# Optimization experiments

Measured on AMD Instinct MI355X. Metric: run time of the kernel, lower is better.

The kernel has to match this reference:

```python
import jax, jax.numpy as jnp
import numpy as np
from jax import lax

B, W, L, E, V, C, H, O = 16384, 5, 20, 50, 100000, 128, 4096, 50


def setup_inputs() -> dict:
    key = jax.random.key(0)
    ks = jax.random.split(key, 10)
    x = jax.random.randint(ks[0], (B, W), 1, V)
    word_id_to_chars_ids = jax.random.randint(ks[1], (V, L), 0, C)
    word_emb = jax.random.normal(ks[2], (V, E), dtype=jnp.float32) * 0.1
    word_emb = word_emb.at[0].set(0.0)  # padding_idx=0
    char_emb = jax.random.normal(ks[3], (C, E), dtype=jnp.float32) * 0.1
    char_emb = char_emb.at[0].set(0.0)  # padding_idx=0
    conv_w = jax.random.normal(ks[4], (E, E, 3), dtype=jnp.float32) * (1.0 / np.sqrt(E * 3))
    conv_b = jax.random.normal(ks[5], (E,), dtype=jnp.float32) * 0.01
    fc1_w = jax.random.normal(ks[6], (H, E * W), dtype=jnp.float32) * (1.0 / np.sqrt(E * W))
    fc1_b = jnp.zeros((H,), dtype=jnp.float32)
    fc2_w = jax.random.normal(ks[7], (O, H), dtype=jnp.float32) * (1.0 / np.sqrt(H))
    fc2_b = jnp.zeros((O,), dtype=jnp.float32)
    return {"x": x, "word_id_to_chars_ids": word_id_to_chars_ids,
            "word_emb": word_emb, "char_emb": char_emb,
            "conv_w": conv_w, "conv_b": conv_b,
            "fc1_w": fc1_w, "fc1_b": fc1_b, "fc2_w": fc2_w, "fc2_b": fc2_b}


def reference(x, word_id_to_chars_ids, word_emb, char_emb, conv_w, conv_b,
              fc1_w, fc1_b, fc2_w, fc2_b):
    # per-window char ids: [B, 5, L] -> char embeddings [B, 5, L, E]
    char_ids = word_id_to_chars_ids[x]
    ce = char_emb[char_ids]
    # conv1d over char positions: reshape to NCW = [B*5, E, L]
    ce = ce.reshape(B * W, L, E).transpose(0, 2, 1)
    conv = lax.conv_general_dilated(ce, conv_w, window_strides=(1,),
                                    padding=[(1, 1)],
                                    dimension_numbers=("NCH", "OIH", "NCH"))
    conv = conv + conv_b[None, :, None]
    # max-pool over char positions (kernel == L): [B*5, E] -> [B, 5, E]
    chars = jnp.max(conv, axis=2).reshape(B, W, E)
    words = word_emb[x]  # [B, 5, E]
    h = (words + chars).reshape(B, W * E)  # view(-1, 250)
    h = jnp.tanh(h @ fc1_w.T + fc1_b)
    logits = h @ fc2_w.T + fc2_b
    return jax.nn.softmax(logits, axis=1)
```

## Files before the change

kernel.cpp:

```cpp
#include <hip/hip_runtime.h>
#include <hip/hip_bf16.h>


typedef __attribute__((ext_vector_type(8))) short short8;
typedef __attribute__((ext_vector_type(4))) float float4v;

__device__ inline short bf16b(float f) {
    __hip_bfloat16 h = __float2bfloat16(f);
    return *reinterpret_cast<short*>(&h);
}
__device__ inline uint packbf2(float a, float b) {
    return (uint)(ushort)bf16b(a) | ((uint)(ushort)bf16b(b) << 16);
}
__device__ inline void gload_lds16(const void* g, void* l) {
    __builtin_amdgcn_global_load_lds(
        (const __attribute__((address_space(1))) unsigned int*)g,
        (__attribute__((address_space(3))) unsigned int*)l, 16, 0, 0);
}

struct F3 { float x, y, z; };

__global__ __launch_bounds__(256) void prep_kernel(
    const float* __restrict__ fc1_w, const float* __restrict__ fc1_b,
    const float* __restrict__ fc2_w, const float* __restrict__ char_emb,
    const float* __restrict__ conv_w, short* __restrict__ wbf,
    short* __restrict__ w2bf, float* __restrict__ gt2,
    __hip_bfloat16* __restrict__ ha)
{
    const int bid = blockIdx.x;
    if (bid < 4096) {
        int idx = bid * 256 + threadIdx.x;
        int n = idx >> 8, k = idx & 255;
        float v = (k < 250) ? fc1_w[n * 250 + k] : (k == 250 ? fc1_b[n] : 0.f);
        int CT = n >> 4, mm = n & 15;
        int ks = k >> 5, qq = (k >> 3) & 3, j = k & 7;
        wbf[((CT * 8 + ks) * 64 + qq * 16 + mm) * 8 + j] = bf16b(v);
    } else if (bid < 5120) {
        int idx = (bid - 4096) * 256 + threadIdx.x;
        int o = idx >> 12, k = idx & 4095;
        float v = (o < 50) ? fc2_w[idx] : 0.f;
        int Ot = o >> 4, mm = o & 15;
        int kst = k >> 5, qq = (k >> 3) & 3, j = k & 7;
        w2bf[((kst * 4 + Ot) * 64 + qq * 16 + mm) * 8 + j] = bf16b(v);
    } else if (bid < 5195) {
        int idx = (bid - 5120) * 256 + threadIdx.x;
        if (idx >= 19200) return;
        int c = idx / 150, rem = idx - c * 150;
        int kk = rem / 50, o = rem - kk * 50;
        const float* ce = char_emb + c * 50;
        const float* w  = conv_w + o * 150 + kk;
        float s = 0.f;
        #pragma unroll 10
        for (int i = 0; i < 50; ++i) s += ce[i] * w[i * 3];
        gt2[(c * 50 + o) * 3 + kk] = s;
    } else {
        int idx = (bid - 5195) * 256 + threadIdx.x;
        int b = idx / 6, j = idx - b * 6;
        ha[b * 256 + 250 + j] = __float2bfloat16(j == 0 ? 1.f : 0.f);
    }
}

__global__ __launch_bounds__(512, 4) void conv_kernel(
    const int* __restrict__ x, const int* __restrict__ wci,
    const float* __restrict__ word_emb, const float* __restrict__ conv_b,
    const float* __restrict__ gt2, __hip_bfloat16* __restrict__ ha)
{
    __shared__ float Gs[19200];
    __shared__ uint  cpack[640];
    __shared__ int   xs[128];
    char* gsb = (char*)Gs;

    const int tid = threadIdx.x;
    const int gw0 = blockIdx.x * 128;

    #pragma unroll
    for (int t = 0; t < 38; ++t) {
        int idx = t * 512 + tid;
        if (idx < 19200) Gs[idx] = gt2[idx];
    }

    if (tid < 128) {
        const int xid = x[gw0 + tid];
        xs[tid] = xid;
        const int* crow = wci + (size_t)xid * 20;
        int cid[20];
        #pragma unroll
        for (int p = 0; p < 20; ++p) cid[p] = crow[p];
        #pragma unroll
        for (int u = 0; u < 5; ++u)
            cpack[tid * 5 + u] = (uint)cid[u * 4] | ((uint)cid[u * 4 + 1] << 8)
                               | ((uint)cid[u * 4 + 2] << 16) | ((uint)cid[u * 4 + 3] << 24);
    }
    __syncthreads();

    const int lane = tid & 63;
    const int wv   = tid >> 6;
    const int oc   = (lane < 50) ? lane : 49;
    const int oc12 = oc * 12;
    const float cbias = conv_b[oc];

    for (int it = 0; it < 16; ++it) {
        const int wl = it * 8 + wv;
        uint cw[5];
        #pragma unroll
        for (int u = 0; u < 5; ++u) cw[u] = cpack[wl * 5 + u];
        const int xid = xs[wl];

        int cb[20];
        #pragma unroll
        for (int p = 0; p < 20; ++p) {
            const int c = (int)((cw[p >> 2] >> ((p & 3) * 8)) & 0xFF);
            cb[p] = c * 600 + oc12;
        }

        F3 r[11];
        #pragma unroll
        for (int l = 0; l < 11; ++l) r[l] = *(const F3*)(gsb + cb[l]);

        float mx = r[0].y + r[1].z;
        #pragma unroll
        for (int l = 1; l < 10; ++l) {
            float s = r[l].y + r[l - 1].x + r[l + 1].z;
            mx = fmaxf(mx, s);
        }
        const F3 r9 = r[9], r10 = r[10];

        F3 qv[9];
        #pragma unroll
        for (int l = 0; l < 9; ++l) qv[l] = *(const F3*)(gsb + cb[11 + l]);

        {
            float s = r10.y + r9.x + qv[0].z;
            mx = fmaxf(mx, s);
        }
        {
            float s = qv[0].y + r10.x + qv[1].z;
            mx = fmaxf(mx, s);
        }
        #pragma unroll
        for (int l = 12; l < 19; ++l) {
            float s = qv[l - 11].y + qv[l - 12].x + qv[l - 10].z;
            mx = fmaxf(mx, s);
        }
        {
            float s = qv[8].y + qv[7].x;
            mx = fmaxf(mx, s);
        }

        const float wer = word_emb[(size_t)xid * 50 + oc];
        const float res = mx + cbias + wer;
        const int gw = gw0 + wl;
        const int b = gw / 5, wp = gw - b * 5;
        if (lane < 50)
            ha[b * 256 + wp * 50 + lane] = __float2bfloat16(res);
    }
}

__global__ __launch_bounds__(512, 1) void fused_kernel(
    const __hip_bfloat16* __restrict__ ha, const short* __restrict__ wbf,
    const short* __restrict__ w2bf, float* __restrict__ gpart)
{
    __shared__ char smem[147456];
    short8* Bsv = (short8*)smem;
    char*   hsb = smem + 131072;
    float*  partf = (float*)smem;

    const int tid  = threadIdx.x;
    const int lane = tid & 63;
    const int wv   = tid >> 6;
    const int wr = wv >> 2, wc = wv & 3;
    const int q = lane >> 4, m = lane & 15;
    const int rg = blockIdx.x >> 1, kh = blockIdx.x & 1;
    const int m0 = rg * 64;
    const int q2base = q >> 1, slot = q & 1;

    const short8* wbfv  = (const short8*)wbf;
    const short8* w2bfv = (const short8*)w2bf;
    const short8* hav   = (const short8*)ha;

    short8 av[2][8];
    #pragma unroll
    for (int mt = 0; mt < 2; ++mt)
        #pragma unroll
        for (int ks = 0; ks < 8; ++ks)
            av[mt][ks] = hav[(size_t)(m0 + wr * 32 + mt * 16 + m) * 32 + ks * 4 + q];
    #pragma unroll
    for (int mt = 0; mt < 2; ++mt)
        #pragma unroll
        for (int ks = 0; ks < 8; ++ks)
            asm volatile("" : "+v"(av[mt][ks]));

    #pragma unroll
    for (int i = 0; i < 8; ++i)
        gload_lds16(wbfv + (size_t)(kh * 16) * 4096 + i * 512 + tid,
                    Bsv + i * 512 + tid);
    __syncthreads();

    float4v acc2[2][4] = {};

    #pragma unroll 4
    for (int chl = 0; chl < 16; ++chl) {
        const int buf = chl & 1;
        const int chg = kh * 16 + chl;

        short8 b2[4];
        #pragma unroll
        for (int Ot = 0; Ot < 4; ++Ot)
            b2[Ot] = w2bfv[(size_t)((chg * 4 + wc) * 4 + Ot) * 64 + lane];

        #pragma unroll
        for (int i = 0; i < 8; ++i)
            gload_lds16(wbfv + (size_t)(chg + 1) * 4096 + i * 512 + tid,
                        Bsv + (buf ^ 1) * 4096 + i * 512 + tid);

        float4v acc[2][2] = {};
        #pragma unroll
        for (int ks = 0; ks < 8; ++ks) {
            short8 bv[2];
            #pragma unroll
            for (int nt = 0; nt < 2; ++nt)
                bv[nt] = Bsv[buf * 4096 + ((wc * 2 + nt) * 8 + ks) * 64 + lane];
            #pragma unroll
            for (int mt = 0; mt < 2; ++mt)
                #pragma unroll
                for (int nt = 0; nt < 2; ++nt)
                    acc[mt][nt] = __builtin_amdgcn_mfma_f32_16x16x32_bf16(
                        bv[nt], av[mt][ks], acc[mt][nt], 0, 0, 0);
        }

        #pragma unroll
        for (int mt = 0; mt < 2; ++mt) {
            const int frag = (wr * 2 + mt) * 4 + wc;
            #pragma unroll
            for (int nt = 0; nt < 2; ++nt) {
                float tv[4];
                #pragma unroll
                for (int r = 0; r < 4; ++r)
                    tv[r] = 1.f - 2.f / (__expf(2.f * acc[mt][nt][r]) + 1.f);
                const int q2 = nt * 2 + q2base;
                const uint p0 = packbf2(tv[0], tv[1]);
                const uint p1 = packbf2(tv[2], tv[3]);
                *(uint2*)(hsb + ((frag * 64 + q2 * 16 + m) * 16 + slot * 8))
                    = make_uint2(p0, p1);
            }
        }

        {
            short8 a2[2];
            #pragma unroll
            for (int mt = 0; mt < 2; ++mt)
                a2[mt] = *(const short8*)(hsb
                    + (((wr * 2 + mt) * 4 + wc) * 64 + lane) * 16);
            #pragma unroll
            for (int mt = 0; mt < 2; ++mt)
                #pragma unroll
                for (int Ot = 0; Ot < 4; ++Ot)
                    acc2[mt][Ot] = __builtin_amdgcn_mfma_f32_16x16x32_bf16(
                        a2[mt], b2[Ot], acc2[mt][Ot], 0, 0, 0);
        }

        __syncthreads();
    }

    #pragma unroll
    for (int mt = 0; mt < 2; ++mt)
        #pragma unroll
        for (int Ot = 0; Ot < 4; ++Ot)
            #pragma unroll
            for (int r = 0; r < 4; ++r)
                partf[(size_t)wc * 4096
                      + ((wr * 2 + mt) * 16 + q * 4 + r) * 64 + Ot * 16 + m]
                    = acc2[mt][Ot][r];
    __syncthreads();

    #pragma unroll
    for (int t = 0; t < 8; ++t) {
        int idx = t * 512 + tid;
        float s = partf[idx] + partf[4096 + idx]
                + partf[8192 + idx] + partf[12288 + idx];
        gpart[(size_t)blockIdx.x * 4096 + idx] = s;
    }
}

__global__ __launch_bounds__(256) void combine_kernel(
    const float* __restrict__ gpart, const float* __restrict__ fc2_b,
    float* __restrict__ out)
{
    const int tid  = threadIdx.x;
    const int lane = tid & 63;
    const int wv   = tid >> 6;
    const float bias = (lane < 50) ? fc2_b[lane] : 0.f;

    #pragma unroll
    for (int rr = 0; rr < 8; ++rr) {
        const int row = blockIdx.x * 32 + wv * 8 + rr;
        const int rg = row >> 6, rl = row & 63;
        float v = gpart[(size_t)(rg * 2) * 4096 + rl * 64 + lane]
                + gpart[(size_t)(rg * 2 + 1) * 4096 + rl * 64 + lane];
        v = (lane < 50) ? v + bias : -1e30f;
        float mx = v;
        #pragma unroll
        for (int off = 32; off > 0; off >>= 1) mx = fmaxf(mx, __shfl_xor(mx, off));
        float e = __expf(v - mx);
        float s = e;
        #pragma unroll
        for (int off = 32; off > 0; off >>= 1) s += __shfl_xor(s, off);
        if (lane < 50)
            out[(size_t)row * 50 + lane] = e / s;
    }
}

extern "C" void kernel_launch(void* const* d_in, const int* in_sizes, int n_in,
                              void* d_out, int out_size, void* d_ws, size_t ws_size,
                              hipStream_t stream) {
    const int*   x        = (const int*)  d_in[0];
    const int*   wci      = (const int*)  d_in[1];
    const float* word_emb = (const float*)d_in[2];
    const float* char_emb = (const float*)d_in[3];
    const float* conv_w   = (const float*)d_in[4];
    const float* conv_b   = (const float*)d_in[5];
    const float* fc1_w    = (const float*)d_in[6];
    const float* fc1_b    = (const float*)d_in[7];
    const float* fc2_w    = (const float*)d_in[8];
    const float* fc2_b    = (const float*)d_in[9];
    float* out = (float*)d_out;

    char* ws = (char*)d_ws;
    __hip_bfloat16* ha  = (__hip_bfloat16*)ws;
    short* wbf   = (short*)(ws + ((size_t)8  << 20));
    short* w2bf  = (short*)(ws + ((size_t)10 << 20));
    float* gt2   = (float*)(ws + ((size_t)11 << 20));
    float* gpart = (float*)(ws + ((size_t)16 << 20));

    prep_kernel<<<5579, 256, 0, stream>>>(fc1_w, fc1_b, fc2_w, char_emb,
                                          conv_w, wbf, w2bf, gt2, ha);
    conv_kernel<<<640, 512, 0, stream>>>(x, wci, word_emb, conv_b, gt2, ha);
    fused_kernel<<<512, 512, 0, stream>>>(ha, wbf, w2bf, gpart);
    combine_kernel<<<512, 256, 0, stream>>>(gpart, fc2_b, out);
}
```

Measured before the change: 205.1 us.

## Fuse char-conv, MLP and softmax into one kernel with full-K blocks

Folds the char-conv/word-embedding stage and the softmax combine into the main MLP kernel. Each block now computes its own 64 rows of the hidden input in LDS, swizzled, instead of round-tripping through global memory. The K-split across two blocks is removed, so each block loops over all 32 hidden chunks and applies bias and softmax locally. The conv table is split into a 2-wide and a 1-wide plane for aligned loads. This cuts two launches and the global intermediates, but halves the grid to 256 blocks and adds a serial conv prologue per block.

```diff
diff --git a/kernel.cpp b/kernel.cpp
--- a/kernel.cpp
+++ b/kernel.cpp
@@ -18,14 +18,11 @@
         (__attribute__((address_space(3))) unsigned int*)l, 16, 0, 0);
 }
 
-struct F3 { float x, y, z; };
-
 __global__ __launch_bounds__(256) void prep_kernel(
     const float* __restrict__ fc1_w, const float* __restrict__ fc1_b,
     const float* __restrict__ fc2_w, const float* __restrict__ char_emb,
     const float* __restrict__ conv_w, short* __restrict__ wbf,
-    short* __restrict__ w2bf, float* __restrict__ gt2,
-    __hip_bfloat16* __restrict__ ha)
+    short* __restrict__ w2bf, float* __restrict__ gt2)
 {
     const int bid = blockIdx.x;
     if (bid < 4096) {
@@ -42,7 +39,7 @@
         int Ot = o >> 4, mm = o & 15;
         int kst = k >> 5, qq = (k >> 3) & 3, j = k & 7;
         w2bf[((kst * 4 + Ot) * 64 + qq * 16 + mm) * 8 + j] = bf16b(v);
-    } else if (bid < 5195) {
+    } else {
         int idx = (bid - 5120) * 256 + threadIdx.x;
         if (idx >= 19200) return;
         int c = idx / 150, rem = idx - c * 150;
@@ -52,156 +49,146 @@
         float s = 0.f;
         #pragma unroll 10
         for (int i = 0; i < 50; ++i) s += ce[i] * w[i * 3];
-        gt2[(c * 50 + o) * 3 + kk] = s;
-    } else {
-        int idx = (bid - 5195) * 256 + threadIdx.x;
-        int b = idx / 6, j = idx - b * 6;
-        ha[b * 256 + 250 + j] = __float2bfloat16(j == 0 ? 1.f : 0.f);
-    }
-}
-
-__global__ __launch_bounds__(512, 4) void conv_kernel(
+        if (kk < 2) gt2[(c * 50 + o) * 2 + kk] = s;
+        else        gt2[12800 + c * 50 + o] = s;
+    }
+}
+
+__global__ __launch_bounds__(512, 1) void fused_kernel(
     const int* __restrict__ x, const int* __restrict__ wci,
     const float* __restrict__ word_emb, const float* __restrict__ conv_b,
-    const float* __restrict__ gt2, __hip_bfloat16* __restrict__ ha)
-{
-    __shared__ float Gs[19200];
-    __shared__ uint  cpack[640];
-    __shared__ int   xs[128];
-    char* gsb = (char*)Gs;
-
-    const int tid = threadIdx.x;
-    const int gw0 = blockIdx.x * 128;
-
-    #pragma unroll
-    for (int t = 0; t < 38; ++t) {
-        int idx = t * 512 + tid;
-        if (idx < 19200) Gs[idx] = gt2[idx];
-    }
-
-    if (tid < 128) {
-        const int xid = x[gw0 + tid];
-        xs[tid] = xid;
-        const int* crow = wci + (size_t)xid * 20;
-        int cid[20];
-        #pragma unroll
-        for (int p = 0; p < 20; ++p) cid[p] = crow[p];
-        #pragma unroll
-        for (int u = 0; u < 5; ++u)
-            cpack[tid * 5 + u] = (uint)cid[u * 4] | ((uint)cid[u * 4 + 1] << 8)
-                               | ((uint)cid[u * 4 + 2] << 16) | ((uint)cid[u * 4 + 3] << 24);
-    }
-    __syncthreads();
-
-    const int lane = tid & 63;
-    const int wv   = tid >> 6;
-    const int oc   = (lane < 50) ? lane : 49;
-    const int oc12 = oc * 12;
-    const float cbias = conv_b[oc];
-
-    for (int it = 0; it < 16; ++it) {
-        const int wl = it * 8 + wv;
-        uint cw[5];
-        #pragma unroll
-        for (int u = 0; u < 5; ++u) cw[u] = cpack[wl * 5 + u];
-        const int xid = xs[wl];
-
-        int cb[20];
-        #pragma unroll
-        for (int p = 0; p < 20; ++p) {
-            const int c = (int)((cw[p >> 2] >> ((p & 3) * 8)) & 0xFF);
-            cb[p] = c * 600 + oc12;
-        }
-
-        F3 r[11];
-        #pragma unroll
-        for (int l = 0; l < 11; ++l) r[l] = *(const F3*)(gsb + cb[l]);
-
-        float mx = r[0].y + r[1].z;
-        #pragma unroll
-        for (int l = 1; l < 10; ++l) {
-            float s = r[l].y + r[l - 1].x + r[l + 1].z;
-            mx = fmaxf(mx, s);
-        }
-        const F3 r9 = r[9], r10 = r[10];
-
-        F3 qv[9];
-        #pragma unroll
-        for (int l = 0; l < 9; ++l) qv[l] = *(const F3*)(gsb + cb[11 + l]);
-
-        {
-            float s = r10.y + r9.x + qv[0].z;
-            mx = fmaxf(mx, s);
-        }
-        {
-            float s = qv[0].y + r10.x + qv[1].z;
-            mx = fmaxf(mx, s);
-        }
-        #pragma unroll
-        for (int l = 12; l < 19; ++l) {
-            float s = qv[l - 11].y + qv[l - 12].x + qv[l - 10].z;
-            mx = fmaxf(mx, s);
-        }
-        {
-            float s = qv[8].y + qv[7].x;
-            mx = fmaxf(mx, s);
-        }
-
-        const float wer = word_emb[(size_t)xid * 50 + oc];
-        const float res = mx + cbias + wer;
-        const int gw = gw0 + wl;
-        const int b = gw / 5, wp = gw - b * 5;
-        if (lane < 50)
-            ha[b * 256 + wp * 50 + lane] = __float2bfloat16(res);
-    }
-}
-
-__global__ __launch_bounds__(512, 1) void fused_kernel(
-    const __hip_bfloat16* __restrict__ ha, const short* __restrict__ wbf,
-    const short* __restrict__ w2bf, float* __restrict__ gpart)
+    const float* __restrict__ gt2, const short* __restrict__ wbf,
+    const short* __restrict__ w2bf, const float* __restrict__ fc2_b,
+    float* __restrict__ out)
 {
     __shared__ char smem[147456];
-    short8* Bsv = (short8*)smem;
-    char*   hsb = smem + 131072;
+    short8* Bsv   = (short8*)smem;
+    char*   hsb   = smem + 131072;
     float*  partf = (float*)smem;
+    char*   gsb   = smem;
+    uint*   cpackS = (uint*)(smem + 76800);
+    int*    xsS    = (int*)(smem + 83200);
+    char*   haS    = smem + 98304;
 
     const int tid  = threadIdx.x;
     const int lane = tid & 63;
     const int wv   = tid >> 6;
     const int wr = wv >> 2, wc = wv & 3;
     const int q = lane >> 4, m = lane & 15;
-    const int rg = blockIdx.x >> 1, kh = blockIdx.x & 1;
-    const int m0 = rg * 64;
+    const int m0 = blockIdx.x * 64;
     const int q2base = q >> 1, slot = q & 1;
 
     const short8* wbfv  = (const short8*)wbf;
     const short8* w2bfv = (const short8*)w2bf;
-    const short8* hav   = (const short8*)ha;
+
+    {
+        const float4* g4 = (const float4*)gt2;
+        float4* s4 = (float4*)gsb;
+        #pragma unroll
+        for (int i = 0; i < 10; ++i) {
+            int idx = i * 512 + tid;
+            if (idx < 4800) s4[idx] = g4[idx];
+        }
+    }
+    if (tid < 320) {
+        const int xid = x[m0 * 5 + tid];
+        xsS[tid] = xid;
+        const int* crow = wci + (size_t)xid * 20;
+        int cid[20];
+        #pragma unroll
+        for (int p = 0; p < 20; ++p) cid[p] = crow[p];
+        #pragma unroll
+        for (int u = 0; u < 5; ++u)
+            cpackS[tid * 5 + u] = (uint)cid[u * 4] | ((uint)cid[u * 4 + 1] << 8)
+                                | ((uint)cid[u * 4 + 2] << 16) | ((uint)cid[u * 4 + 3] << 24);
+    }
+    __syncthreads();
+
+    {
+        const int oc = (lane < 50) ? lane : 49;
+        const float cbias = conv_b[oc];
+        const int oc8 = oc * 8, oc4 = oc * 4;
+        for (int i = 0; i < 40; ++i) {
+            const int w = i * 8 + wv;
+            const int xid = xsS[w];
+            const float wer = word_emb[(size_t)xid * 50 + oc];
+            uint cw[5];
+            #pragma unroll
+            for (int u = 0; u < 5; ++u) cw[u] = cpackS[w * 5 + u];
+            int cc[20];
+            #pragma unroll
+            for (int p = 0; p < 20; ++p)
+                cc[p] = (int)((cw[p >> 2] >> ((p & 3) * 8)) & 0xFF);
+
+            float2 r01[11]; float r2[11];
+            #pragma unroll
+            for (int l = 0; l < 11; ++l) {
+                r01[l] = *(const float2*)(gsb + cc[l] * 400 + oc8);
+                r2[l]  = *(const float*)(gsb + 51200 + cc[l] * 200 + oc4);
+            }
+            float mx = r01[0].y + r2[1];
+            #pragma unroll
+            for (int l = 1; l < 10; ++l) {
+                float s = r01[l].y + r01[l - 1].x + r2[l + 1];
+                mx = fmaxf(mx, s);
+            }
+            const float2 r9 = r01[9], r10 = r01[10];
+
+            float2 q01[9]; float q2v[9];
+            #pragma unroll
+            for (int l = 0; l < 9; ++l) {
+                q01[l] = *(const float2*)(gsb + cc[11 + l] * 400 + oc8);
+                q2v[l] = *(const float*)(gsb + 51200 + cc[11 + l] * 200 + oc4);
+            }
+            { float s = r10.y + r9.x + q2v[0];  mx = fmaxf(mx, s); }
+            { float s = q01[0].y + r10.x + q2v[1]; mx = fmaxf(mx, s); }
+            #pragma unroll
+            for (int l = 12; l < 19; ++l) {
+                float s = q01[l - 11].y + q01[l - 12].x + q2v[l - 10];
+                mx = fmaxf(mx, s);
+            }
+            { float s = q01[8].y + q01[7].x; mx = fmaxf(mx, s); }
+
+            if (lane < 50) {
+                const int s = w / 5, wp = w - s * 5;
+                const int byteoff = (s * 512 + (wp * 50 + oc) * 2) ^ ((s & 7) << 4);
+                *(short*)(haS + byteoff) = bf16b(mx + cbias + wer);
+            }
+        }
+    }
+    if (tid < 384) {
+        const int s = tid / 6, j = tid - s * 6;
+        const int byteoff = (s * 512 + (250 + j) * 2) ^ ((s & 7) << 4);
+        *(short*)(haS + byteoff) = bf16b(j == 0 ? 1.f : 0.f);
+    }
+    __syncthreads();
 
     short8 av[2][8];
     #pragma unroll
     for (int mt = 0; mt < 2; ++mt)
         #pragma unroll
-        for (int ks = 0; ks < 8; ++ks)
-            av[mt][ks] = hav[(size_t)(m0 + wr * 32 + mt * 16 + m) * 32 + ks * 4 + q];
+        for (int ks = 0; ks < 8; ++ks) {
+            const int r = wr * 32 + mt * 16 + m;
+            const int byteoff = (r * 512 + ks * 64 + q * 16) ^ ((r & 7) << 4);
+            av[mt][ks] = *(const short8*)(haS + byteoff);
+        }
     #pragma unroll
     for (int mt = 0; mt < 2; ++mt)
         #pragma unroll
         for (int ks = 0; ks < 8; ++ks)
             asm volatile("" : "+v"(av[mt][ks]));
+    __syncthreads();
 
     #pragma unroll
     for (int i = 0; i < 8; ++i)
-        gload_lds16(wbfv + (size_t)(kh * 16) * 4096 + i * 512 + tid,
-                    Bsv + i * 512 + tid);
+        gload_lds16(wbfv + i * 512 + tid, Bsv + i * 512 + tid);
     __syncthreads();
 
     float4v acc2[2][4] = {};
 
     #pragma unroll 4
-    for (int chl = 0; chl < 16; ++chl) {
-        const int buf = chl & 1;
-        const int chg = kh * 16 + chl;
+    for (int chg = 0; chg < 32; ++chg) {
+        const int buf = chg & 1;
 
         short8 b2[4];
         #pragma unroll
@@ -276,28 +263,17 @@
     #pragma unroll
     for (int t = 0; t < 8; ++t) {
         int idx = t * 512 + tid;
-        float s = partf[idx] + partf[4096 + idx]
-                + partf[8192 + idx] + partf[12288 + idx];
-        gpart[(size_t)blockIdx.x * 4096 + idx] = s;
-    }
-}
-
-__global__ __launch_bounds__(256) void combine_kernel(
-    const float* __restrict__ gpart, const float* __restrict__ fc2_b,
-    float* __restrict__ out)
-{
-    const int tid  = threadIdx.x;
-    const int lane = tid & 63;
-    const int wv   = tid >> 6;
-    const float bias = (lane < 50) ? fc2_b[lane] : 0.f;
+        int col = idx & 63;
+        float lg = partf[idx] + partf[4096 + idx]
+                 + partf[8192 + idx] + partf[12288 + idx];
+        partf[idx] = (col < 50) ? lg + fc2_b[col] : -1e30f;
+    }
+    __syncthreads();
 
     #pragma unroll
     for (int rr = 0; rr < 8; ++rr) {
-        const int row = blockIdx.x * 32 + wv * 8 + rr;
-        const int rg = row >> 6, rl = row & 63;
-        float v = gpart[(size_t)(rg * 2) * 4096 + rl * 64 + lane]
-                + gpart[(size_t)(rg * 2 + 1) * 4096 + rl * 64 + lane];
-        v = (lane < 50) ? v + bias : -1e30f;
+        const int row = wv * 8 + rr;
+        float v = partf[row * 64 + lane];
         float mx = v;
         #pragma unroll
         for (int off = 32; off > 0; off >>= 1) mx = fmaxf(mx, __shfl_xor(mx, off));
@@ -306,7 +282,7 @@
         #pragma unroll
         for (int off = 32; off > 0; off >>= 1) s += __shfl_xor(s, off);
         if (lane < 50)
-            out[(size_t)row * 50 + lane] = e / s;
+            out[(size_t)(m0 + row) * 50 + lane] = e / s;
     }
 }
 
@@ -326,15 +302,12 @@
     float* out = (float*)d_out;
 
     char* ws = (char*)d_ws;
-    __hip_bfloat16* ha  = (__hip_bfloat16*)ws;
-    short* wbf   = (short*)(ws + ((size_t)8  << 20));
-    short* w2bf  = (short*)(ws + ((size_t)10 << 20));
-    float* gt2   = (float*)(ws + ((size_t)11 << 20));
-    float* gpart = (float*)(ws + ((size_t)16 << 20));
-
-    prep_kernel<<<5579, 256, 0, stream>>>(fc1_w, fc1_b, fc2_w, char_emb,
-                                          conv_w, wbf, w2bf, gt2, ha);
-    conv_kernel<<<640, 512, 0, stream>>>(x, wci, word_emb, conv_b, gt2, ha);
-    fused_kernel<<<512, 512, 0, stream>>>(ha, wbf, w2bf, gpart);
-    combine_kernel<<<512, 256, 0, stream>>>(gpart, fc2_b, out);
-}
+    short* wbf  = (short*)(ws + ((size_t)8  << 20));
+    short* w2bf = (short*)(ws + ((size_t)10 << 20));
+    float* gt2  = (float*)(ws + ((size_t)11 << 20));
+
+    prep_kernel<<<5195, 256, 0, stream>>>(fc1_w, fc1_b, fc2_w, char_emb,
+                                          conv_w, wbf, w2bf, gt2);
+    fused_kernel<<<256, 512, 0, stream>>>(x, wci, word_emb, conv_b, gt2,
+                                          wbf, w2bf, fc2_b, out);
+}
```

Result: faster. 193.0 us (-5.9%).
